# Kernel tuning notes

Hardware: AMD Instinct MI355X
Metric: run time of the kernel (lower is better)

Reference implementation:

```python
import jax, jax.numpy as jnp
import numpy as np

B, NQ, NKV = 2, 1024, 4096
DQ = 1024          # query_dim == context_dim
H, DH = 16, 64     # heads, dim_head
INNER = H * DH     # 1024
SCALE = DH ** -0.5


def setup_inputs() -> dict:
    key = jax.random.key(0)
    ks = jax.random.split(key, 6)
    s = 1.0 / np.sqrt(DQ)
    return {
        "x": jax.random.normal(ks[0], (B, NQ, DQ), dtype=jnp.float32),
        "context": jax.random.normal(ks[1], (B, NKV, DQ), dtype=jnp.float32),
        "Wq": jax.random.normal(ks[2], (DQ, INNER), dtype=jnp.float32) * s,
        "Wkv": jax.random.normal(ks[3], (DQ, 2 * INNER), dtype=jnp.float32) * s,
        "Wout": jax.random.normal(ks[4], (INNER, DQ), dtype=jnp.float32) * (1.0 / np.sqrt(INNER)),
        "b_out": jax.random.normal(ks[5], (DQ,), dtype=jnp.float32) * 0.01,
    }


def _split_heads(t):
    # b n (h d) -> b h n d
    b, n, _ = t.shape
    return t.reshape(b, n, H, DH).transpose(0, 2, 1, 3)


def reference(x, context, Wq, Wkv, Wout, b_out):
    q = x @ Wq                       # [B, NQ, INNER]
    kv = context @ Wkv               # [B, NKV, 2*INNER]
    k, v = jnp.split(kv, 2, axis=-1)
    q, k, v = map(_split_heads, (q, k, v))          # [B, H, n, DH]
    sim = jnp.einsum("bhid,bhjd->bhij", q, k) * SCALE  # [B, H, NQ, NKV]
    attn = jax.nn.softmax(sim, axis=-1)
    out = jnp.einsum("bhij,bhjd->bhid", attn, v)       # [B, H, NQ, DH]
    out = out.transpose(0, 2, 1, 3).reshape(B, NQ, INNER)  # (b h) n d -> b n (h d)
    return out @ Wout + b_out
```

## Files before the change

### kernel.cpp

```cpp
#include <hip/hip_runtime.h>
#include <stdint.h>

#define B_    2
#define NQ_   1024
#define NKV_  4096
#define DQ_   1024
#define H_    16
#define DH_   64
#define INNER_ 1024

typedef unsigned short u16;
typedef uint32_t u32;
typedef __bf16 bf16x8 __attribute__((ext_vector_type(8)));
typedef float  f32x4  __attribute__((ext_vector_type(4)));

__device__ __forceinline__ u16 f2bf(float x) {
  union { float f; uint32_t u; } v; v.f = x;
  uint32_t r = v.u + 0x7FFFu + ((v.u >> 16) & 1u);
  return (u16)(r >> 16);
}
__device__ __forceinline__ u32 pack2(float a, float b) {
  return (u32)f2bf(a) | ((u32)f2bf(b) << 16);
}
__device__ __forceinline__ u32 pack2rn(float a, float b) {
  union { float f; u32 u; } x, y; x.f = a; y.f = b;
  return __builtin_amdgcn_perm(y.u + 0x8000u, x.u + 0x8000u, 0x07060302u);
}
__device__ __forceinline__ float bf2f(u16 s) {
  union { float f; uint32_t u; } v; v.u = ((uint32_t)s) << 16; return v.f;
}

__device__ __forceinline__ void gload16(const void* g, void* l) {
  __builtin_amdgcn_global_load_lds((const __attribute__((address_space(1))) void*)g,
                                   (__attribute__((address_space(3))) void*)l,
                                   16, 0, 0);
}

__global__ __launch_bounds__(256) void prep(const float* __restrict__ x,
                                            const float* __restrict__ ctx,
                                            const float* __restrict__ Wq,
                                            const float* __restrict__ Wkv,
                                            const float* __restrict__ Wout,
                                            u16* __restrict__ xb,
                                            u16* __restrict__ ctxb,
                                            u16* __restrict__ WqT,
                                            u16* __restrict__ WkvT,
                                            u16* __restrict__ WoutT) {
  int bid = blockIdx.x;
  if (bid < 1280) {
    const float* src; u16* dst; int fbase;
    if (bid < 256) { src = x;   dst = xb;   fbase = bid * 2048; }
    else           { src = ctx; dst = ctxb; fbase = (bid - 256) * 2048; }
#pragma unroll
    for (int u = 0; u < 8; ++u) {
      int i = (fbase + u * 256 + threadIdx.x) * 4;
      float4 v = *(const float4*)(src + i);
      uint2 o; o.x = pack2(v.x, v.y); o.y = pack2(v.z, v.w);
      *(uint2*)(dst + i) = o;
    }
    return;
  }
  __shared__ float tile[32][33];
  const float* W; u16* Wt; int K, N, local, nsh;
  int b2 = bid - 1280;
  if (b2 < 1024)      { W = Wq;   Wt = WqT;   K = 1024; N = 1024; local = b2;        nsh = 5; }
  else if (b2 < 3072) { W = Wkv;  Wt = WkvT;  K = 1024; N = 2048; local = b2 - 1024; nsh = 6; }
  else                { W = Wout; Wt = WoutT; K = 1024; N = 1024; local = b2 - 3072; nsh = 5; }
  int n0 = (local & ((1 << nsh) - 1)) * 32;
  int k0 = (local >> nsh) * 32;
  int tx = threadIdx.x & 31, ty = threadIdx.x >> 5;
  for (int i = ty; i < 32; i += 8)
    tile[i][tx] = W[(size_t)(k0 + i) * N + n0 + tx];
  __syncthreads();
  for (int i = ty; i < 32; i += 8)
    Wt[(size_t)(n0 + i) * K + k0 + tx] = f2bf(tile[tx][i]);
}

__global__ __launch_bounds__(512, 2) void kv_gemm(const u16* __restrict__ ctxb,
                                                  const u16* __restrict__ WkvT,
                                                  u16* __restrict__ kb,
                                                  u16* __restrict__ vTb) {
  __shared__ __align__(16) u16 As[2][256 * 64];
  __shared__ __align__(16) u16 Bs[2][256 * 64];
  const int tid = threadIdx.x;
  const int lane = tid & 63;
  const int w = tid >> 6;
  const int wr = w >> 2, wc = w & 3;
  const int l15 = lane & 15, quad = lane >> 4;
  const int K = 1024;

  int bid = blockIdx.x;
  int wgid = (bid & 7) * 32 + (bid >> 3);
  const int tm = wgid >> 3, tn = wgid & 7;
  const int m0 = tm * 256, n0 = tn * 256;
  const u16* Ag = ctxb + (size_t)m0 * K;
  const u16* Bg = WkvT + (size_t)n0 * K;

  size_t offA[2][2], offB[2][2];
#pragma unroll
  for (int ah = 0; ah < 2; ++ah)
#pragma unroll
    for (int p = 0; p < 2; ++p) {
      int c = p * 512 + (w << 6) + lane;
      int s = ah * 128 + (c >> 3);
      int col = ((c & 7) ^ (s & 7)) << 3;
      int rA = ((s >> 6) & 1) * 128 + ((s >> 7) & 1) * 64 + (s & 63);
      int rB = ((s >> 5) & 3) * 64 + ((s >> 7) & 1) * 32 + (s & 31);
      offA[ah][p] = (size_t)rA * 1024 + col;
      offB[ah][p] = (size_t)rB * 1024 + col;
    }

#define STAGE_A(bufi, ah, kk) do { \
    gload16(Ag + offA[ah][0] + (kk), &As[bufi][(ah) * 8192 + (w << 9)]); \
    gload16(Ag + offA[ah][1] + (kk), &As[bufi][(ah) * 8192 + 4096 + (w << 9)]); \
  } while (0)
#define STAGE_B(bufi, bh, kk) do { \
    gload16(Bg + offB[bh][0] + (kk), &Bs[bufi][(bh) * 8192 + (w << 9)]); \
    gload16(Bg + offB[bh][1] + (kk), &Bs[bufi][(bh) * 8192 + 4096 + (w << 9)]); \
  } while (0)
#define LDA2(dst, i8, bufi) do { \
    const int _s = ((i8) >> 2) * 128 + wr * 64 + ((i8) & 3) * 16 + l15; \
    const u16* _p = &As[bufi][_s * 64]; const int _x = _s & 7; \
    dst[0] = *(const bf16x8*)&_p[(quad ^ _x) << 3]; \
    dst[1] = *(const bf16x8*)&_p[((quad + 4) ^ _x) << 3]; \
  } while (0)
#define LDB2(dst, j, bufi) do { \
    const int _s = ((j) >> 1) * 128 + wc * 32 + ((j) & 1) * 16 + l15; \
    const u16* _p = &Bs[bufi][_s * 64]; const int _x = _s & 7; \
    dst[0] = *(const bf16x8*)&_p[(quad ^ _x) << 3]; \
    dst[1] = *(const bf16x8*)&_p[((quad + 4) ^ _x) << 3]; \
  } while (0)
#define MF(i0, j0, bb) do { \
    _Pragma("unroll") \
    for (int _i = 0; _i < 4; ++_i) { \
      acc[(i0) + _i][(j0)    ] = __builtin_amdgcn_mfma_f32_16x16x32_bf16(a[_i][0], bb[0][0], acc[(i0) + _i][(j0)    ], 0, 0, 0); \
      acc[(i0) + _i][(j0)    ] = __builtin_amdgcn_mfma_f32_16x16x32_bf16(a[_i][1], bb[0][1], acc[(i0) + _i][(j0)    ], 0, 0, 0); \
      acc[(i0) + _i][(j0) + 1] = __builtin_amdgcn_mfma_f32_16x16x32_bf16(a[_i][0], bb[1][0], acc[(i0) + _i][(j0) + 1], 0, 0, 0); \
      acc[(i0) + _i][(j0) + 1] = __builtin_amdgcn_mfma_f32_16x16x32_bf16(a[_i][1], bb[1][1], acc[(i0) + _i][(j0) + 1], 0, 0, 0); \
    } \
  } while (0)

  f32x4 acc[8][4] = {};
  bf16x8 a[4][2], b[2][2], c2[2][2];

  STAGE_A(0, 0, 0);
  STAGE_B(0, 0, 0);
  STAGE_B(0, 1, 0);
  STAGE_A(0, 1, 0);
  asm volatile("s_waitcnt vmcnt(4)" ::: "memory");
  __builtin_amdgcn_s_barrier();

#define KTILE(cur, nxt, kk, STG, W1, W2) do { \
     \
    LDB2(b[0], 0, cur); LDB2(b[1], 1, cur); \
    LDA2(a[0], 0, cur); LDA2(a[1], 1, cur); LDA2(a[2], 2, cur); LDA2(a[3], 3, cur); \
    if (STG) STAGE_A(nxt, 0, kk); \
    __builtin_amdgcn_s_barrier(); \
    asm volatile("s_waitcnt lgkmcnt(0)" ::: "memory"); \
    __builtin_amdgcn_s_setprio(1); MF(0, 0, b); __builtin_amdgcn_s_setprio(0); \
    asm volatile("s_waitcnt " W1 ::: "memory"); \
    __builtin_amdgcn_s_barrier(); \
     \
    LDB2(c2[0], 2, cur); LDB2(c2[1], 3, cur); \
    if (STG) STAGE_B(nxt, 0, kk); \
    __builtin_amdgcn_s_barrier(); \
    asm volatile("s_waitcnt lgkmcnt(0)" ::: "memory"); \
    __builtin_amdgcn_s_setprio(1); MF(0, 2, c2); __builtin_amdgcn_s_setprio(0); \
    asm volatile("s_waitcnt " W2 ::: "memory"); \
    __builtin_amdgcn_s_barrier(); \
     \
    LDA2(a[0], 4, cur); LDA2(a[1], 5, cur); LDA2(a[2], 6, cur); LDA2(a[3], 7, cur); \
    if (STG) STAGE_B(nxt, 1, kk); \
    __builtin_amdgcn_s_barrier(); \
    asm volatile("s_waitcnt lgkmcnt(0)" ::: "memory"); \
    __builtin_amdgcn_s_setprio(1); MF(4, 0, b); __builtin_amdgcn_s_setprio(0); \
    __builtin_amdgcn_s_barrier(); \
     \
    if (STG) STAGE_A(nxt, 1, kk); \
    __builtin_amdgcn_s_barrier(); \
    __builtin_amdgcn_s_setprio(1); MF(4, 2, c2); __builtin_amdgcn_s_setprio(0); \
    if (STG) { asm volatile("s_waitcnt vmcnt(4)" ::: "memory"); } \
    __builtin_amdgcn_s_barrier(); \
  } while (0)

  for (int T = 0; T < 15; ++T) {
    const int cur = T & 1, nxt = cur ^ 1, kk = (T + 1) * 64;
    KTILE(cur, nxt, kk, 1, "vmcnt(4)", "vmcnt(4)");
  }
  KTILE(1, 0, 0, 0, "vmcnt(2)", "vmcnt(0)");

  if (tn < 4) {
#pragma unroll
    for (int i8 = 0; i8 < 8; ++i8)
#pragma unroll
      for (int j = 0; j < 4; ++j) {
        int col = n0 + wc * 64 + j * 16 + l15;
#pragma unroll
        for (int r = 0; r < 4; ++r) {
          int row = m0 + wr * 128 + i8 * 16 + quad * 4 + r;
          kb[(size_t)row * 1024 + col] = f2bf(acc[i8][j][r]);
        }
      }
  } else {
    const int bb_ = m0 >> 12;
#pragma unroll
    for (int i8 = 0; i8 < 8; ++i8) {
      int kvr = (m0 & 4095) + wr * 128 + i8 * 16 + quad * 4;
#pragma unroll
      for (int j = 0; j < 4; ++j) {
        int c = (n0 - 1024) + wc * 64 + j * 16 + l15;
        int h = c >> 6, dh = c & 63;
        uint2 st;
        st.x = pack2(acc[i8][j][0], acc[i8][j][1]);
        st.y = pack2(acc[i8][j][2], acc[i8][j][3]);
        *(uint2*)&vTb[((size_t)((bb_ * 16 + h) * 64 + dh)) * NKV_ + kvr] = st;
      }
    }
  }
#undef STAGE_A
#undef STAGE_B
#undef LDA2
#undef LDB2
#undef MF
#undef KTILE
}

__global__ __launch_bounds__(256) void q_gemm(const u16* __restrict__ A,
                                              const u16* __restrict__ Bt,
                                              u16* __restrict__ outp) {
  __shared__ __align__(16) u16 As[64 * 32];
  __shared__ __align__(16) u16 Bs[128 * 32];
  const int tid = threadIdx.x;
  const int lane = tid & 63;
  const int w = tid >> 6;
  const int wr = w >> 1, wc = w & 1;
  const int l15 = lane & 15, quad = lane >> 4;
  const int unit = blockIdx.x;
  const int m0 = (unit >> 3) * 64, n0 = (unit & 7) * 128;
  const int K = 1024, N = 1024;

  const u16* Ab = A + (size_t)m0 * K;
  const u16* Bb = Bt + (size_t)n0 * K;
  f32x4 acc[2][4] = {};

  const int ar = tid >> 2, ac = (tid & 3) << 3;
  const int q1 = w * 64 + lane, q2 = q1 + 256;
  const int br1 = q1 >> 2, bc1 = (q1 & 3) << 3;
  const int br2 = q2 >> 2, bc2 = (q2 & 3) << 3;

  for (int k0 = 0; k0 < K; k0 += 32) {
    __syncthreads();
    gload16(Ab + (size_t)ar * K + k0 + ac, &As[w * 512]);
    gload16(Bb + (size_t)br1 * K + k0 + bc1, &Bs[w * 512]);
    gload16(Bb + (size_t)br2 * K + k0 + bc2, &Bs[2048 + w * 512]);
    __syncthreads();
    bf16x8 af[2], bfr[4];
#pragma unroll
    for (int i = 0; i < 2; ++i)
      af[i] = *(const bf16x8*)&As[(wr * 32 + i * 16 + l15) * 32 + quad * 8];
#pragma unroll
    for (int j = 0; j < 4; ++j)
      bfr[j] = *(const bf16x8*)&Bs[(wc * 64 + j * 16 + l15) * 32 + quad * 8];
#pragma unroll
    for (int i = 0; i < 2; ++i)
#pragma unroll
      for (int j = 0; j < 4; ++j)
        acc[i][j] = __builtin_amdgcn_mfma_f32_16x16x32_bf16(af[i], bfr[j], acc[i][j], 0, 0, 0);
  }

#pragma unroll
  for (int i = 0; i < 2; ++i)
#pragma unroll
    for (int j = 0; j < 4; ++j) {
      int col = n0 + wc * 64 + j * 16 + l15;
#pragma unroll
      for (int r = 0; r < 4; ++r) {
        int row = m0 + wr * 32 + i * 16 + quad * 4 + r;
        outp[(size_t)row * N + col] = f2bf(acc[i][j][r]);
      }
    }
}

__global__ __launch_bounds__(256) void out_gemm(const u16* __restrict__ A,
                                                const u16* __restrict__ Bt,
                                                float* __restrict__ Cout,
                                                const float* __restrict__ bias) {
  __shared__ __align__(16) u16 As[64 * 32];
  __shared__ __align__(16) u16 Bs[128 * 32];
  const int tid = threadIdx.x;
  const int lane = tid & 63;
  const int w = tid >> 6;
  const int wr = w >> 1, wc = w & 1;
  const int l15 = lane & 15, quad = lane >> 4;
  const int unit = blockIdx.x;
  const int m0 = (unit >> 3) * 64, n0 = (unit & 7) * 128;
  const int K = 1024, N = 1024;

  const u16* Ab = A + (size_t)m0 * K;
  const u16* Bb = Bt + (size_t)n0 * K;
  f32x4 acc[2][4] = {};

  const int ar = tid >> 2, ac = (tid & 3) << 3;
  const int q1 = w * 64 + lane, q2 = q1 + 256;
  const int br1 = q1 >> 2, bc1 = (q1 & 3) << 3;
  const int br2 = q2 >> 2, bc2 = (q2 & 3) << 3;

  for (int k0 = 0; k0 < K; k0 += 32) {
    __syncthreads();
    gload16(Ab + (size_t)ar * K + k0 + ac, &As[w * 512]);
    gload16(Bb + (size_t)br1 * K + k0 + bc1, &Bs[w * 512]);
    gload16(Bb + (size_t)br2 * K + k0 + bc2, &Bs[2048 + w * 512]);
    __syncthreads();
    bf16x8 af[2], bfr[4];
#pragma unroll
    for (int i = 0; i < 2; ++i)
      af[i] = *(const bf16x8*)&As[(wr * 32 + i * 16 + l15) * 32 + quad * 8];
#pragma unroll
    for (int j = 0; j < 4; ++j)
      bfr[j] = *(const bf16x8*)&Bs[(wc * 64 + j * 16 + l15) * 32 + quad * 8];
#pragma unroll
    for (int i = 0; i < 2; ++i)
#pragma unroll
      for (int j = 0; j < 4; ++j)
        acc[i][j] = __builtin_amdgcn_mfma_f32_16x16x32_bf16(af[i], bfr[j], acc[i][j], 0, 0, 0);
  }

#pragma unroll
  for (int i = 0; i < 2; ++i)
#pragma unroll
    for (int j = 0; j < 4; ++j) {
      int col = n0 + wc * 64 + j * 16 + l15;
      float bv = bias[col];
#pragma unroll
      for (int r = 0; r < 4; ++r) {
        int row = m0 + wr * 32 + i * 16 + quad * 4 + r;
        Cout[(size_t)row * N + col] = acc[i][j][r] + bv;
      }
    }
}

__global__ __launch_bounds__(256, 3) void attn_kernel(const u16* __restrict__ qg,
                                                      const u16* __restrict__ kb,
                                                      const u16* __restrict__ vT,
                                                      u16* __restrict__ attn_out) {
  __shared__ __align__(16) u16 Ks[128 * 64];
  __shared__ __align__(16) u16 Vs[64 * 128];
  __shared__ __align__(16) u32 P32[4 * 2 * 16 * 20];
  __shared__ float Lr[4][2][16];

  const int tid = threadIdx.x;
  const int lane = tid & 63;
  const int w = tid >> 6;
  const int l15 = lane & 15, quad = lane >> 4;
  const int bh = blockIdx.x, b = bh >> 4, h = bh & 15;
  const int q0 = blockIdx.y * 32;

  const float SC = 0.125f * 1.44269504088896340736f;
  union { u16 s[8]; bf16x8 v; } qf[2][2];
#pragma unroll
  for (int t = 0; t < 2; ++t)
#pragma unroll
    for (int kc = 0; kc < 2; ++kc) {
      const u16* qp = qg + (size_t)(b * NQ_ + q0 + t * 16 + l15) * INNER_ + h * 64 +
                      kc * 32 + quad * 8;
      union { u16 s[8]; uint4 u; } tmp;
      tmp.u = *(const uint4*)qp;
#pragma unroll
      for (int e = 0; e < 8; ++e) qf[t][kc].s[e] = f2bf(bf2f(tmp.s[e]) * SC);
    }

#define STAGEKV(j0) do { \
    _Pragma("unroll") \
    for (int i_ = 0; i_ < 4; ++i_) { \
      int s_ = i_ * 256 + tid; \
      int kr = s_ >> 3, kg = (s_ ^ kr) & 7; \
      gload16(kb + (size_t)(b * NKV_ + (j0) + kr) * 1024 + h * 64 + kg * 8, \
              &Ks[(i_ * 256 + w * 64) * 8]); \
      int vr = s_ >> 4, vg = (s_ ^ vr) & 15; \
      gload16(vT + (size_t)(bh * 64 + vr) * NKV_ + (j0) + vg * 8, \
              &Vs[(i_ * 256 + w * 64) * 8]); \
    } \
  } while (0)

  f32x4 Oacc[4][2] = {};
  float l_lane[2] = {0.f, 0.f};

  STAGEKV(0);

  for (int it = 0; it < 32; ++it) {
    __syncthreads();

    bf16x8 kf[2][2];
#pragma unroll
    for (int kvt = 0; kvt < 2; ++kvt)
#pragma unroll
      for (int kc = 0; kc < 2; ++kc)
        kf[kvt][kc] = *(const bf16x8*)
          &Ks[(w * 32 + kvt * 16 + l15) * 64 + (((kc * 4 + quad) ^ l15) & 7) * 8];
    bf16x8 vf[4];
#pragma unroll
    for (int d = 0; d < 4; ++d)
      vf[d] = *(const bf16x8*)
        &Vs[(d * 16 + l15) * 128 + (((w * 4 + quad) ^ l15) & 15) * 8];

    __syncthreads();

    if (it < 31) STAGEKV((it + 1) * 128);

    f32x4 sacc[2][2] = {};
    __builtin_amdgcn_s_setprio(1);
#pragma unroll
    for (int kvt = 0; kvt < 2; ++kvt)
#pragma unroll
      for (int t = 0; t < 2; ++t)
#pragma unroll
        for (int kc = 0; kc < 2; ++kc)
          sacc[kvt][t] = __builtin_amdgcn_mfma_f32_16x16x32_bf16(
              kf[kvt][kc], qf[t][kc].v, sacc[kvt][t], 0, 0, 0);
    __builtin_amdgcn_s_setprio(0);

#pragma unroll
    for (int kvt = 0; kvt < 2; ++kvt)
#pragma unroll
      for (int t = 0; t < 2; ++t) {
        float p0 = __builtin_amdgcn_exp2f(sacc[kvt][t][0]);
        float p1 = __builtin_amdgcn_exp2f(sacc[kvt][t][1]);
        float p2 = __builtin_amdgcn_exp2f(sacc[kvt][t][2]);
        float p3 = __builtin_amdgcn_exp2f(sacc[kvt][t][3]);
        l_lane[t] += (p0 + p1) + (p2 + p3);
        uint2 pk; pk.x = pack2rn(p0, p1); pk.y = pack2rn(p2, p3);
        *(uint2*)&P32[((w * 2 + t) * 16 + l15) * 20 + kvt * 8 + quad * 2] = pk;
      }

    bf16x8 pf[2];
#pragma unroll
    for (int t = 0; t < 2; ++t)
      pf[t] = *(const bf16x8*)&P32[((w * 2 + t) * 16 + l15) * 20 + quad * 4];
    __builtin_amdgcn_s_setprio(1);
#pragma unroll
    for (int d = 0; d < 4; ++d)
#pragma unroll
      for (int t = 0; t < 2; ++t)
        Oacc[d][t] = __builtin_amdgcn_mfma_f32_16x16x32_bf16(vf[d], pf[t], Oacc[d][t],
                                                             0, 0, 0);
    __builtin_amdgcn_s_setprio(0);
  }
#undef STAGEKV

#pragma unroll
  for (int t = 0; t < 2; ++t) {
    l_lane[t] += __shfl_xor(l_lane[t], 16);
    l_lane[t] += __shfl_xor(l_lane[t], 32);
  }
  if (quad == 0) {
#pragma unroll
    for (int t = 0; t < 2; ++t) Lr[w][t][l15] = l_lane[t];
  }
  __syncthreads();
  const int tw = w & 1;
  float inv = 1.0f / (Lr[0][tw][l15] + Lr[1][tw][l15] + Lr[2][tw][l15] + Lr[3][tw][l15]);

  float* red = (float*)P32;
  u16* ob = attn_out + (size_t)(b * NQ_ + q0 + tw * 16 + l15) * INNER_ + h * 64;
#pragma unroll
  for (int d = 0; d < 4; ++d) {
    __syncthreads();
#pragma unroll
    for (int t = 0; t < 2; ++t)
      *(f32x4*)&red[(w * 2 + t) * 256 + quad * 64 + l15 * 4] = Oacc[d][t];
    __syncthreads();
    if (w < 2) {
      f32x4 r = *(const f32x4*)&red[(0 * 2 + w) * 256 + quad * 64 + l15 * 4];
#pragma unroll
      for (int ww = 1; ww < 4; ++ww) {
        f32x4 c = *(const f32x4*)&red[(ww * 2 + w) * 256 + quad * 64 + l15 * 4];
        r[0] += c[0]; r[1] += c[1]; r[2] += c[2]; r[3] += c[3];
      }
      *(u32*)(ob + d * 16 + quad * 4)     = pack2(r[0] * inv, r[1] * inv);
      *(u32*)(ob + d * 16 + quad * 4 + 2) = pack2(r[2] * inv, r[3] * inv);
    }
  }
}

extern "C" void kernel_launch(void* const* d_in, const int* in_sizes, int n_in,
                              void* d_out, int out_size, void* d_ws, size_t ws_size,
                              hipStream_t stream) {
  const float* x    = (const float*)d_in[0];
  const float* ctx  = (const float*)d_in[1];
  const float* Wq   = (const float*)d_in[2];
  const float* Wkv  = (const float*)d_in[3];
  const float* Wout = (const float*)d_in[4];
  const float* bout = (const float*)d_in[5];

  char* ws = (char*)d_ws;
  u16* xb    = (u16*)(ws + (size_t)( 0u << 20));
  u16* ab    = (u16*)(ws + (size_t)( 0u << 20));
  u16* ctxb  = (u16*)(ws + (size_t)( 4u << 20));
  u16* WqT   = (u16*)(ws + (size_t)(20u << 20));
  u16* WkvT  = (u16*)(ws + (size_t)(22u << 20));
  u16* WoutT = (u16*)(ws + (size_t)(26u << 20));
  u16* qb    = (u16*)(ws + (size_t)(28u << 20));
  u16* kb    = (u16*)(ws + (size_t)(32u << 20));
  u16* vTb   = (u16*)(ws + (size_t)(48u << 20));

  prep<<<5376, 256, 0, stream>>>(x, ctx, Wq, Wkv, Wout, xb, ctxb, WqT, WkvT, WoutT);
  q_gemm<<<256, 256, 0, stream>>>(xb, WqT, qb);
  kv_gemm<<<256, 512, 0, stream>>>(ctxb, WkvT, kb, vTb);
  attn_kernel<<<dim3(32, 32), 256, 0, stream>>>(qb, kb, vTb, ab);
  out_gemm<<<256, 256, 0, stream>>>(ab, WoutT, (float*)d_out, bout);
}
```

Before: 244.5 us.

## Widen attention block to 128 queries so each staged KV tile is reused by 4x more rows

The attention kernel now runs 512 threads per block: four warp groups each own 32 query rows, and two halves split each 128-key KV tile. One block therefore covers 128 queries instead of 32, so every K/V tile staged into shared memory serves four times as many query rows, cutting global and L2 traffic for K/V. The final reduction merges only the two key-halves instead of four warps. The trade-offs are a larger P buffer in shared memory, more registers per thread, and a grid of 256 blocks, which may leave CUs underoccupied.

```diff
diff --git a/kernel.cpp b/kernel.cpp
--- a/kernel.cpp
+++ b/kernel.cpp
@@ -339,21 +339,22 @@
     }
 }
 
-__global__ __launch_bounds__(256, 3) void attn_kernel(const u16* __restrict__ qg,
+__global__ __launch_bounds__(512, 2) void attn_kernel(const u16* __restrict__ qg,
                                                       const u16* __restrict__ kb,
                                                       const u16* __restrict__ vT,
                                                       u16* __restrict__ attn_out) {
   __shared__ __align__(16) u16 Ks[128 * 64];
   __shared__ __align__(16) u16 Vs[64 * 128];
-  __shared__ __align__(16) u32 P32[4 * 2 * 16 * 20];
-  __shared__ float Lr[4][2][16];
+  __shared__ __align__(16) u32 P32[8 * 2 * 16 * 36];
+  __shared__ float Lr[8][2][16];
 
   const int tid = threadIdx.x;
   const int lane = tid & 63;
   const int w = tid >> 6;
+  const int wq = w & 3, wk = w >> 2;
   const int l15 = lane & 15, quad = lane >> 4;
   const int bh = blockIdx.x, b = bh >> 4, h = bh & 15;
-  const int q0 = blockIdx.y * 32;
+  const int q0 = blockIdx.y * 128 + wq * 32;
 
   const float SC = 0.125f * 1.44269504088896340736f;
   union { u16 s[8]; bf16x8 v; } qf[2][2];
@@ -371,14 +372,14 @@
 
 #define STAGEKV(j0) do { \
     _Pragma("unroll") \
-    for (int i_ = 0; i_ < 4; ++i_) { \
-      int s_ = i_ * 256 + tid; \
+    for (int i_ = 0; i_ < 2; ++i_) { \
+      int s_ = i_ * 512 + tid; \
       int kr = s_ >> 3, kg = (s_ ^ kr) & 7; \
       gload16(kb + (size_t)(b * NKV_ + (j0) + kr) * 1024 + h * 64 + kg * 8, \
-              &Ks[(i_ * 256 + w * 64) * 8]); \
+              &Ks[(i_ * 512 + w * 64) * 8]); \
       int vr = s_ >> 4, vg = (s_ ^ vr) & 15; \
       gload16(vT + (size_t)(bh * 64 + vr) * NKV_ + (j0) + vg * 8, \
-              &Vs[(i_ * 256 + w * 64) * 8]); \
+              &Vs[(i_ * 512 + w * 64) * 8]); \
     } \
   } while (0)
 
@@ -390,59 +391,61 @@
   for (int it = 0; it < 32; ++it) {
     __syncthreads();
 
-    bf16x8 kf[2][2];
-#pragma unroll
-    for (int kvt = 0; kvt < 2; ++kvt)
+    bf16x8 kf[4][2];
+#pragma unroll
+    for (int kvt = 0; kvt < 4; ++kvt)
 #pragma unroll
       for (int kc = 0; kc < 2; ++kc)
         kf[kvt][kc] = *(const bf16x8*)
-          &Ks[(w * 32 + kvt * 16 + l15) * 64 + (((kc * 4 + quad) ^ l15) & 7) * 8];
-    bf16x8 vf[4];
+          &Ks[(wk * 64 + kvt * 16 + l15) * 64 + (((kc * 4 + quad) ^ l15) & 7) * 8];
+    bf16x8 vf[4][2];
 #pragma unroll
     for (int d = 0; d < 4; ++d)
-      vf[d] = *(const bf16x8*)
-        &Vs[(d * 16 + l15) * 128 + (((w * 4 + quad) ^ l15) & 15) * 8];
+#pragma unroll
+      for (int kh = 0; kh < 2; ++kh)
+        vf[d][kh] = *(const bf16x8*)
+          &Vs[(d * 16 + l15) * 128 + (((wk * 8 + kh * 4 + quad) ^ l15) & 15) * 8];
 
     __syncthreads();
 
     if (it < 31) STAGEKV((it + 1) * 128);
 
-    f32x4 sacc[2][2] = {};
-    __builtin_amdgcn_s_setprio(1);
-#pragma unroll
-    for (int kvt = 0; kvt < 2; ++kvt)
-#pragma unroll
-      for (int t = 0; t < 2; ++t)
-#pragma unroll
-        for (int kc = 0; kc < 2; ++kc)
-          sacc[kvt][t] = __builtin_amdgcn_mfma_f32_16x16x32_bf16(
-              kf[kvt][kc], qf[t][kc].v, sacc[kvt][t], 0, 0, 0);
-    __builtin_amdgcn_s_setprio(0);
-
-#pragma unroll
-    for (int kvt = 0; kvt < 2; ++kvt)
+#pragma unroll
+    for (int kvt = 0; kvt < 4; ++kvt) {
+      f32x4 sacc[2] = {};
+      __builtin_amdgcn_s_setprio(1);
 #pragma unroll
       for (int t = 0; t < 2; ++t) {
-        float p0 = __builtin_amdgcn_exp2f(sacc[kvt][t][0]);
-        float p1 = __builtin_amdgcn_exp2f(sacc[kvt][t][1]);
-        float p2 = __builtin_amdgcn_exp2f(sacc[kvt][t][2]);
-        float p3 = __builtin_amdgcn_exp2f(sacc[kvt][t][3]);
+        sacc[t] = __builtin_amdgcn_mfma_f32_16x16x32_bf16(kf[kvt][0], qf[t][0].v, sacc[t], 0, 0, 0);
+        sacc[t] = __builtin_amdgcn_mfma_f32_16x16x32_bf16(kf[kvt][1], qf[t][1].v, sacc[t], 0, 0, 0);
+      }
+      __builtin_amdgcn_s_setprio(0);
+#pragma unroll
+      for (int t = 0; t < 2; ++t) {
+        float p0 = __builtin_amdgcn_exp2f(sacc[t][0]);
+        float p1 = __builtin_amdgcn_exp2f(sacc[t][1]);
+        float p2 = __builtin_amdgcn_exp2f(sacc[t][2]);
+        float p3 = __builtin_amdgcn_exp2f(sacc[t][3]);
         l_lane[t] += (p0 + p1) + (p2 + p3);
         uint2 pk; pk.x = pack2rn(p0, p1); pk.y = pack2rn(p2, p3);
-        *(uint2*)&P32[((w * 2 + t) * 16 + l15) * 20 + kvt * 8 + quad * 2] = pk;
-      }
-
-    bf16x8 pf[2];
+        *(uint2*)&P32[((w * 2 + t) * 16 + l15) * 36 + kvt * 8 + quad * 2] = pk;
+      }
+    }
+
+    bf16x8 pf[2][2];
 #pragma unroll
     for (int t = 0; t < 2; ++t)
-      pf[t] = *(const bf16x8*)&P32[((w * 2 + t) * 16 + l15) * 20 + quad * 4];
+#pragma unroll
+      for (int kh = 0; kh < 2; ++kh)
+        pf[t][kh] = *(const bf16x8*)&P32[((w * 2 + t) * 16 + l15) * 36 + kh * 16 + quad * 4];
     __builtin_amdgcn_s_setprio(1);
 #pragma unroll
     for (int d = 0; d < 4; ++d)
 #pragma unroll
-      for (int t = 0; t < 2; ++t)
-        Oacc[d][t] = __builtin_amdgcn_mfma_f32_16x16x32_bf16(vf[d], pf[t], Oacc[d][t],
-                                                             0, 0, 0);
+      for (int t = 0; t < 2; ++t) {
+        Oacc[d][t] = __builtin_amdgcn_mfma_f32_16x16x32_bf16(vf[d][0], pf[t][0], Oacc[d][t], 0, 0, 0);
+        Oacc[d][t] = __builtin_amdgcn_mfma_f32_16x16x32_bf16(vf[d][1], pf[t][1], Oacc[d][t], 0, 0, 0);
+      }
     __builtin_amdgcn_s_setprio(0);
   }
 #undef STAGEKV
@@ -457,27 +460,29 @@
     for (int t = 0; t < 2; ++t) Lr[w][t][l15] = l_lane[t];
   }
   __syncthreads();
-  const int tw = w & 1;
-  float inv = 1.0f / (Lr[0][tw][l15] + Lr[1][tw][l15] + Lr[2][tw][l15] + Lr[3][tw][l15]);
-
-  float* red = (float*)P32;
-  u16* ob = attn_out + (size_t)(b * NQ_ + q0 + tw * 16 + l15) * INNER_ + h * 64;
-#pragma unroll
-  for (int d = 0; d < 4; ++d) {
-    __syncthreads();
-#pragma unroll
-    for (int t = 0; t < 2; ++t)
-      *(f32x4*)&red[(w * 2 + t) * 256 + quad * 64 + l15 * 4] = Oacc[d][t];
-    __syncthreads();
-    if (w < 2) {
-      f32x4 r = *(const f32x4*)&red[(0 * 2 + w) * 256 + quad * 64 + l15 * 4];
-#pragma unroll
-      for (int ww = 1; ww < 4; ++ww) {
-        f32x4 c = *(const f32x4*)&red[(ww * 2 + w) * 256 + quad * 64 + l15 * 4];
+
+  float* RedF = (float*)P32;
+  if (wk == 1) {
+#pragma unroll
+    for (int d = 0; d < 4; ++d)
+#pragma unroll
+      for (int t = 0; t < 2; ++t)
+        *(f32x4*)&RedF[(((w & 3) * 4 + d) * 2 + t) * 256 + lane * 4] = Oacc[d][t];
+  }
+  __syncthreads();
+  if (wk == 0) {
+#pragma unroll
+    for (int t = 0; t < 2; ++t) {
+      float inv = 1.0f / (Lr[w][t][l15] + Lr[w + 4][t][l15]);
+      u16* ob = attn_out + (size_t)(b * NQ_ + q0 + t * 16 + l15) * INNER_ + h * 64;
+#pragma unroll
+      for (int d = 0; d < 4; ++d) {
+        f32x4 r = Oacc[d][t];
+        f32x4 c = *(const f32x4*)&RedF[((w * 4 + d) * 2 + t) * 256 + lane * 4];
         r[0] += c[0]; r[1] += c[1]; r[2] += c[2]; r[3] += c[3];
-      }
-      *(u32*)(ob + d * 16 + quad * 4)     = pack2(r[0] * inv, r[1] * inv);
-      *(u32*)(ob + d * 16 + quad * 4 + 2) = pack2(r[2] * inv, r[3] * inv);
+        *(u32*)(ob + d * 16 + quad * 4)     = pack2(r[0] * inv, r[1] * inv);
+        *(u32*)(ob + d * 16 + quad * 4 + 2) = pack2(r[2] * inv, r[3] * inv);
+      }
     }
   }
 }
@@ -506,6 +511,6 @@
   prep<<<5376, 256, 0, stream>>>(x, ctx, Wq, Wkv, Wout, xb, ctxb, WqT, WkvT, WoutT);
   q_gemm<<<256, 256, 0, stream>>>(xb, WqT, qb);
   kv_gemm<<<256, 512, 0, stream>>>(ctxb, WkvT, kb, vTb);
-  attn_kernel<<<dim3(32, 32), 256, 0, stream>>>(qb, kb, vTb, ab);
+  attn_kernel<<<dim3(32, 8), 512, 0, stream>>>(qb, kb, vTb, ab);
   out_gemm<<<256, 256, 0, stream>>>(ab, WoutT, (float*)d_out, bout);
 }
```

Measured after the change: 229.6 us. -6.1%, faster.
